# Performance work log

Measured on AMD Instinct MI355X. Metric: run time of the kernel, lower is better.

Reference implementation:

```python
import jax, jax.numpy as jnp
import numpy as np

D_MODEL = 1024
N_HEADS = 16
HEAD_DIM = D_MODEL // N_HEADS
B, S = 2, 2048


def setup_inputs() -> dict:
    key = jax.random.key(0)
    ks = jax.random.split(key, 6)
    w_scale = 1.0 / np.sqrt(D_MODEL)
    return {
        "query": jax.random.normal(ks[0], (B, S, D_MODEL), dtype=jnp.float32),
        "Wq": jax.random.normal(ks[1], (D_MODEL, D_MODEL), dtype=jnp.float32) * w_scale,
        "Wk": jax.random.normal(ks[2], (D_MODEL, D_MODEL), dtype=jnp.float32) * w_scale,
        "Wv": jax.random.normal(ks[3], (D_MODEL, D_MODEL), dtype=jnp.float32) * w_scale,
        "Wo": jax.random.normal(ks[4], (D_MODEL, D_MODEL), dtype=jnp.float32) * w_scale,
        "bo": jnp.zeros((D_MODEL,), dtype=jnp.float32),
    }


def reference(query, Wq, Wk, Wv, Wo, bo):
    # Self-attention: key = value = query (forward() defaults).
    b, t, _ = query.shape
    # Q/K/V projections (nn.Linear applies x @ W.T; weights here are stored as
    # [out, in] like torch, so project with W.T). Split into heads: [B,H,T,Dh].
    def proj(x, W):
        return (x @ W.T).reshape(b, t, N_HEADS, HEAD_DIM).transpose(0, 2, 1, 3)

    q = proj(query, Wq)
    k = proj(query, Wk)
    v = proj(query, Wv)

    scale = 1.0 / np.sqrt(HEAD_DIM)
    scores = jnp.einsum("bhqd,bhkd->bhqk", q, k) * scale  # [B,H,T,T]
    # Causal mask (is_causal=True, not cross-attention).
    causal = jnp.tril(jnp.ones((t, t), dtype=bool))
    scores = jnp.where(causal, scores, jnp.finfo(scores.dtype).min)
    weights = jax.nn.softmax(scores, axis=-1)
    out = jnp.einsum("bhqk,bhkd->bhqd", weights, v)  # [B,H,T,Dh]
    out = out.transpose(0, 2, 1, 3).reshape(b, t, D_MODEL)
    # Output projection with bias (dropout is identity in eval mode).
    return out @ Wo.T + bo
```

## Files before the change

### kernel.cpp

```cpp
#include <hip/hip_runtime.h>
#include <hip/hip_bf16.h>
#include <math.h>

typedef __attribute__((ext_vector_type(8))) short short8;
typedef __attribute__((ext_vector_type(4))) float floatx4;
typedef __attribute__((ext_vector_type(2))) _Float16 half2v;
typedef __attribute__((ext_vector_type(4))) _Float16 half4v;

#define MFMA_BF16_32(a, b, c) __builtin_amdgcn_mfma_f32_16x16x32_bf16(a, b, c, 0, 0, 0)
#define MFMA_F16_16(a, b, c) __builtin_amdgcn_mfma_f32_16x16x16f16(a, b, c, 0, 0, 0)

#define PIPE_BAR4() asm volatile("s_waitcnt vmcnt(4)\n\ts_barrier" ::: "memory")
#define PIPE_BAR0() asm volatile("s_waitcnt vmcnt(0)\n\ts_barrier" ::: "memory")

static constexpr int NH = 16;
static constexpr int Bb = 2;
static constexpr int Ss = 2048;
static constexpr int DM = 1024;

__device__ inline unsigned short f2bf(float f) {
    unsigned int u = __float_as_uint(f);
    u += 0x7fffu + ((u >> 16) & 1u);
    return (unsigned short)(u >> 16);
}

__device__ __forceinline__ half2v pkrtz(float a, float b) {
    return __builtin_bit_cast(half2v, __builtin_amdgcn_cvt_pkrtz(a, b));
}

__device__ __forceinline__ void gload_lds16(const unsigned short* g, unsigned short* l) {
    __builtin_amdgcn_global_load_lds(
        (const __attribute__((address_space(1))) unsigned int*)g,
        (__attribute__((address_space(3))) unsigned int*)l, 16, 0, 0);
}

__global__ void convert_all(const float* __restrict__ X, const float* __restrict__ w0,
                            const float* __restrict__ w1, const float* __restrict__ w2,
                            const float* __restrict__ w3, unsigned short* __restrict__ dstX,
                            unsigned short* __restrict__ dstW) {
    const int bid = blockIdx.x;
    const float* src;
    unsigned short* dst;
    int i;
    if (bid < 4096) {
        src = X; dst = dstX; i = bid * 256 + threadIdx.x;
    } else {
        const int w = (bid - 4096) >> 10;
        src = (w == 0) ? w0 : (w == 1) ? w1 : (w == 2) ? w2 : w3;
        dst = dstW + (size_t)w * 1048576;
        i = ((bid - 4096) & 1023) * 256 + threadIdx.x;
    }
    float4 v = ((const float4*)src)[i];
    ushort4 o;
    o.x = f2bf(v.x); o.y = f2bf(v.y); o.z = f2bf(v.z); o.w = f2bf(v.w);
    ((ushort4*)dst)[i] = o;
}

__global__ __launch_bounds__(256) void gemm_qkv(const unsigned short* __restrict__ A,
                                                const unsigned short* __restrict__ Bm,
                                                unsigned short* __restrict__ Qp,
                                                unsigned short* __restrict__ Kp,
                                                unsigned short* __restrict__ Vt) {
    __shared__ __align__(16) unsigned short As[2][4096];
    __shared__ __align__(16) unsigned short Bs[2][4096];
    const int K = 1024;
    const int tid = threadIdx.x;
    const int wave = tid >> 6, lane = tid & 63;
    const int quad = lane >> 4, l16 = lane & 15;
    const int wr = wave >> 1, wc = wave & 1;

    const int l = blockIdx.x;
    const int xcd = l & 7, slot = l >> 3;
    const int bx = (xcd & 3) * 8 + (slot & 7);
    const int by = (xcd >> 2) * 12 + (slot >> 3);
    const int bm = bx * 128;
    const int bn = by * 128;

    const int s0 = wave * 64 + lane;
    const int srow = s0 >> 2;
    const int scg = (s0 & 3) ^ ((srow >> 1) & 3);
    const unsigned short* gA0 = A + (size_t)(bm + srow) * K + scg * 8;
    const unsigned short* gB0 = Bm + (size_t)(bn + srow) * K + scg * 8;

    auto stage = [&](int k0, int buf) {
        gload_lds16(gA0 + k0, &As[buf][wave * 512]);
        gload_lds16(gA0 + (size_t)64 * K + k0, &As[buf][2048 + wave * 512]);
        gload_lds16(gB0 + k0, &Bs[buf][wave * 512]);
        gload_lds16(gB0 + (size_t)64 * K + k0, &Bs[buf][2048 + wave * 512]);
    };

    floatx4 acc[4][4];
#pragma unroll
    for (int i = 0; i < 4; i++)
#pragma unroll
        for (int j = 0; j < 4; j++) acc[i][j] = (floatx4)0.0f;

    stage(0, 0);
    int buf = 0;
    for (int k0 = 0; k0 < K; k0 += 32) {
        __syncthreads();
        if (k0 + 32 < K) stage(k0 + 32, buf ^ 1);
        short8 af[4];
#pragma unroll
        for (int im = 0; im < 4; im++) {
            const int frow = wr * 64 + im * 16 + l16;
            af[im] = *(const short8*)&As[buf][frow * 32 + ((quad ^ ((frow >> 1) & 3)) * 8)];
        }
#pragma unroll
        for (int jn = 0; jn < 4; jn++) {
            const int frow = wc * 64 + jn * 16 + l16;
            short8 bf = *(const short8*)&Bs[buf][frow * 32 + ((quad ^ ((frow >> 1) & 3)) * 8)];
#pragma unroll
            for (int im = 0; im < 4; im++) acc[im][jn] = MFMA_BF16_32(af[im], bf, acc[im][jn]);
        }
        buf ^= 1;
    }
    __syncthreads();

    unsigned short* LB = &As[0][0];

    if (by < 16) {
        unsigned short* dst = (by < 8) ? Qp : Kp;
        const int nb = (by & 7) * 128;
        const float scale = (by < 8) ? 0.125f : 1.0f;
#pragma unroll
        for (int hf = 0; hf < 2; ++hf) {
            if (wc == hf) {
#pragma unroll
                for (int im = 0; im < 4; im++)
#pragma unroll
                    for (int jn = 0; jn < 4; jn++) {
                        const int row = wr * 64 + im * 16 + quad * 4;
                        const int col = jn * 16 + l16;
#pragma unroll
                        for (int r = 0; r < 4; r++)
                            LB[(row + r) * 64 + col] = f2bf(acc[im][jn][r] * scale);
                    }
            }
            __syncthreads();
#pragma unroll
            for (int i = 0; i < 4; ++i) {
                const int flat = i * 256 + tid;
                const int row = flat >> 3, ch = flat & 7;
                short8 v = *(const short8*)&LB[row * 64 + ch * 8];
                *(short8*)&dst[(size_t)(bm + row) * 1024 + nb + hf * 64 + ch * 8] = v;
            }
            __syncthreads();
        }
    } else {
        _Float16* LF = (_Float16*)LB;
        const int dbase = (by - 16) * 128;
        const int bI = bm >> 11, sbase = bm & 2047;
#pragma unroll
        for (int hf = 0; hf < 2; ++hf) {
            if (wc == hf) {
#pragma unroll
                for (int im = 0; im < 4; im++)
#pragma unroll
                    for (int jn = 0; jn < 4; jn++) {
                        const int d64 = jn * 16 + l16;
                        const int sl = wr * 64 + im * 16 + quad * 4;
                        *(half2v*)&LF[d64 * 128 + sl] = pkrtz(acc[im][jn][0], acc[im][jn][1]);
                        *(half2v*)&LF[d64 * 128 + sl + 2] = pkrtz(acc[im][jn][2], acc[im][jn][3]);
                    }
            }
            __syncthreads();
#pragma unroll
            for (int i = 0; i < 4; ++i) {
                const int flat = i * 256 + tid;
                const int dr = flat >> 4, ch = flat & 15;
                short8 v = *(const short8*)&LF[dr * 128 + ch * 8];
                const int d = dbase + hf * 64 + dr;
                const int head = d >> 6, d64g = d & 63;
                *(short8*)&Vt[(((size_t)(bI * 16 + head)) * 64 + d64g) * 2048 + sbase + ch * 8] = v;
            }
            __syncthreads();
        }
    }
}

__global__ __launch_bounds__(256) void gemm_out(const unsigned short* __restrict__ A,
                                                const unsigned short* __restrict__ Bm,
                                                float* __restrict__ C,
                                                const float* __restrict__ bias) {
    __shared__ __align__(16) unsigned short As[2][8192];
    __shared__ __align__(16) unsigned short Bs[2][4096];
    const int K = 1024;
    const int tid = threadIdx.x;
    const int wave = tid >> 6, lane = tid & 63;
    const int quad = lane >> 4, l16 = lane & 15;

    const int l = blockIdx.x;
    const int xcd = l & 7, slot = l >> 3;
    const int bx = (xcd & 3) * 8 + (slot & 7);
    const int by = (xcd >> 2) * 8 + (slot >> 3);
    const int bm = bx * 128, bn = by * 64;

    const int s0 = wave * 64 + lane;
    const int srow = s0 >> 2;
    const int scg = (s0 & 3) ^ ((srow >> 1) & 3);
    const unsigned short* gA0 = A + (size_t)(bm + srow) * K + scg * 8;
    const unsigned short* gB0 = Bm + (size_t)(bn + srow) * K + scg * 8;

    auto stage = [&](int k0, int buf) {
#pragma unroll
        for (int kh = 0; kh < 2; ++kh) {
            gload_lds16(gA0 + k0 + kh * 32, &As[buf][kh * 4096 + wave * 512]);
            gload_lds16(gA0 + (size_t)64 * K + k0 + kh * 32,
                        &As[buf][kh * 4096 + 2048 + wave * 512]);
            gload_lds16(gB0 + k0 + kh * 32, &Bs[buf][kh * 2048 + wave * 512]);
        }
    };

    floatx4 acc[2][4];
#pragma unroll
    for (int i = 0; i < 2; i++)
#pragma unroll
        for (int j = 0; j < 4; j++) acc[i][j] = (floatx4)0.0f;

    stage(0, 0);
    int buf = 0;
    for (int k0 = 0; k0 < K; k0 += 64) {
        __syncthreads();
        if (k0 + 64 < K) stage(k0 + 64, buf ^ 1);
#pragma unroll
        for (int kh = 0; kh < 2; ++kh) {
            const int abase = kh * 4096, bbase = kh * 2048;
            short8 af[2];
#pragma unroll
            for (int im = 0; im < 2; im++) {
                const int frow = wave * 32 + im * 16 + l16;
                af[im] = *(const short8*)&As[buf][abase + frow * 32 +
                                                  ((quad ^ ((frow >> 1) & 3)) * 8)];
            }
#pragma unroll
            for (int jn = 0; jn < 4; jn++) {
                const int frow = jn * 16 + l16;
                short8 bf = *(const short8*)&Bs[buf][bbase + frow * 32 +
                                                     ((quad ^ ((frow >> 1) & 3)) * 8)];
#pragma unroll
                for (int im = 0; im < 2; im++) acc[im][jn] = MFMA_BF16_32(af[im], bf, acc[im][jn]);
            }
        }
        buf ^= 1;
    }

#pragma unroll
    for (int im = 0; im < 2; im++) {
#pragma unroll
        for (int jn = 0; jn < 4; jn++) {
            const int row0 = bm + wave * 32 + im * 16 + quad * 4;
            const int colg = bn + jn * 16 + l16;
            const float bv = bias[colg];
#pragma unroll
            for (int r = 0; r < 4; r++)
                C[(size_t)(row0 + r) * 1024 + colg] = acc[im][jn][r] + bv;
        }
    }
}

__global__ __launch_bounds__(256) void flash_attn(const unsigned short* __restrict__ Qp,
                                                  const unsigned short* __restrict__ Kp,
                                                  const _Float16* __restrict__ Vt,
                                                  unsigned short* __restrict__ Out) {
    __shared__ __align__(16) unsigned short Ks[3][4096];
    __shared__ __align__(16) _Float16 Vs[3][4096];
    const int lin = blockIdx.x;
    const int xcd = lin & 7, slot = lin >> 3;
    const int pair = xcd * 4 + ((slot >> 4) & 3);
    const int h = pair & 15, b = pair >> 4;
    const int qt0 = slot & 15;
    const int qt = ((slot >> 5) & 1) ? 15 - qt0 : qt0;

    const int tid = threadIdx.x, w = tid >> 6, lane = tid & 63;
    const int quad = lane >> 4, l16 = lane & 15;

    short8 qfA[2], qfB[2];
    {
        const unsigned short* qa =
            Qp + ((size_t)(b * 2048 + qt * 128 + w * 16 + l16) << 10) + h * 64 + quad * 8;
        qfA[0] = *(const short8*)qa;
        qfA[1] = *(const short8*)(qa + 32);
        const unsigned short* qb = qa + ((size_t)64 << 10);
        qfB[0] = *(const short8*)qb;
        qfB[1] = *(const short8*)(qb + 32);
    }

    const int t8 = tid >> 3;
    const int cg = (tid & 7) ^ (t8 & 7);
    const unsigned short* gK0 = Kp + ((size_t)(b * 2048 + t8) << 10) + h * 64 + cg * 8;
    const unsigned short* gK1 = gK0 + ((size_t)32 << 10);
    const _Float16* gV0 = Vt + ((size_t)((b * 16 + h) * 64 + t8) << 11) + cg * 8;
    const _Float16* gV1 = gV0 + ((size_t)32 << 11);
    unsigned short* ldsK = &Ks[0][0] + w * 512;
    _Float16* ldsV = &Vs[0][0] + w * 512;

    auto stage = [&](int kt, int buf) {
        const size_t ko = (size_t)kt << 16;
        const size_t vo = (size_t)kt << 6;
        gload_lds16(gK0 + ko, ldsK + buf * 4096);
        gload_lds16(gK1 + ko, ldsK + buf * 4096 + 2048);
        gload_lds16((const unsigned short*)(gV0 + vo), (unsigned short*)(ldsV + buf * 4096));
        gload_lds16((const unsigned short*)(gV1 + vo), (unsigned short*)(ldsV + buf * 4096 + 2048));
    };

    const int ktEnd = 2 * qt + 1;
    stage(0, 0);
    stage(1, 1);

    floatx4 accA[4], accB[4];
#pragma unroll
    for (int dt = 0; dt < 4; dt++) { accA[dt] = (floatx4)0.0f; accB[dt] = (floatx4)0.0f; }
    float lA = 0.0f, lB = 0.0f;
    const int qloc = w * 16 + l16;
    const int sw = l16 & 7;

    int buf = 0;
    for (int kt = 0; kt <= ktEnd; ++kt) {
        if (kt < ktEnd) { PIPE_BAR4(); } else { PIPE_BAR0(); }
        const int nbuf = (buf == 2) ? 0 : buf + 1;
        const int pbuf = (nbuf == 2) ? 0 : nbuf + 1;
        if (kt + 2 <= ktEnd) stage(kt + 2, pbuf);
        const bool aAct = (kt <= 2 * qt);
        const bool aDiag = (kt == 2 * qt);
        const bool bDiag = (kt == ktEnd);
        const unsigned short* KB = &Ks[buf][0];
        const _Float16* VB = &Vs[buf][0];

#pragma unroll
        for (int sc = 0; sc < 4; ++sc) {
            const int rowk = sc * 16 + l16;
            short8 kf0 = *(const short8*)&KB[rowk * 64 + ((quad ^ sw) * 8)];
            short8 kf1 = *(const short8*)&KB[rowk * 64 + (((4 + quad) ^ sw) * 8)];

            half4v pA, pB;
            if (aAct) {
                floatx4 sA = MFMA_BF16_32(kf0, qfA[0], (floatx4)(-2.0f));
                sA = MFMA_BF16_32(kf1, qfA[1], sA);
                float ps[4];
#pragma unroll
                for (int r = 0; r < 4; ++r) {
                    float e = __expf(sA[r]);
                    if (aDiag && (sc * 16 + quad * 4 + r > qloc)) e = 0.0f;
                    ps[r] = e;
                }
                lA += (ps[0] + ps[1]) + (ps[2] + ps[3]);
                pA = __builtin_shufflevector(pkrtz(ps[0], ps[1]), pkrtz(ps[2], ps[3]), 0, 1, 2, 3);
            }
            {
                floatx4 sB = MFMA_BF16_32(kf0, qfB[0], (floatx4)(-2.0f));
                sB = MFMA_BF16_32(kf1, qfB[1], sB);
                float ps[4];
#pragma unroll
                for (int r = 0; r < 4; ++r) {
                    float e = __expf(sB[r]);
                    if (bDiag && (sc * 16 + quad * 4 + r > qloc)) e = 0.0f;
                    ps[r] = e;
                }
                lB += (ps[0] + ps[1]) + (ps[2] + ps[3]);
                pB = __builtin_shufflevector(pkrtz(ps[0], ps[1]), pkrtz(ps[2], ps[3]), 0, 1, 2, 3);
            }

#pragma unroll
            for (int dt = 0; dt < 4; ++dt) {
                const int rowv = dt * 16 + l16;
                const int cgv = ((sc * 2 + (quad >> 1)) ^ sw);
                half4v vf = *(const half4v*)&VB[rowv * 64 + cgv * 8 + (quad & 1) * 4];
                if (aAct) accA[dt] = MFMA_F16_16(vf, pA, accA[dt]);
                accB[dt] = MFMA_F16_16(vf, pB, accB[dt]);
            }
        }
        buf = nbuf;
    }

    lA += __shfl_xor(lA, 16); lA += __shfl_xor(lA, 32);
    lB += __shfl_xor(lB, 16); lB += __shfl_xor(lB, 32);
    const float iA = 1.0f / lA;
    const float iB = 1.0f / lB;

    const size_t rowA = (size_t)(b * 2048 + qt * 128 + w * 16 + l16);
    const size_t rowB = rowA + 64;
#pragma unroll
    for (int dt = 0; dt < 4; ++dt) {
        const int col = h * 64 + dt * 16 + quad * 4;
        ushort4 oa, ob;
        oa.x = f2bf(accA[dt][0] * iA); oa.y = f2bf(accA[dt][1] * iA);
        oa.z = f2bf(accA[dt][2] * iA); oa.w = f2bf(accA[dt][3] * iA);
        ob.x = f2bf(accB[dt][0] * iB); ob.y = f2bf(accB[dt][1] * iB);
        ob.z = f2bf(accB[dt][2] * iB); ob.w = f2bf(accB[dt][3] * iB);
        *(ushort4*)&Out[rowA * 1024 + col] = oa;
        *(ushort4*)&Out[rowB * 1024 + col] = ob;
    }
}

extern "C" void kernel_launch(void* const* d_in, const int* in_sizes, int n_in,
                              void* d_out, int out_size, void* d_ws, size_t ws_size,
                              hipStream_t stream) {
    const float* X  = (const float*)d_in[0];
    const float* Wq = (const float*)d_in[1];
    const float* Wk = (const float*)d_in[2];
    const float* Wv = (const float*)d_in[3];
    const float* Wo = (const float*)d_in[4];
    const float* bo = (const float*)d_in[5];

    unsigned short* ws = (unsigned short*)d_ws;
    unsigned short* Xb   = ws;
    unsigned short* W4   = ws + (size_t)4194304;
    unsigned short* Wob  = W4 + (size_t)3145728;
    unsigned short* Qp   = ws + (size_t)8388608;
    unsigned short* Kp   = ws + (size_t)12582912;
    unsigned short* Vt   = ws + (size_t)16777216;
    unsigned short* At   = ws + (size_t)20971520;

    convert_all<<<8192, 256, 0, stream>>>(X, Wq, Wk, Wv, Wo, Xb, W4);

    gemm_qkv<<<768, 256, 0, stream>>>(Xb, W4, Qp, Kp, Vt);

    flash_attn<<<512, 256, 0, stream>>>(Qp, Kp, (const _Float16*)Vt, At);

    gemm_out<<<512, 256, 0, stream>>>(At, Wob, (float*)d_out, bo);
}
```

Measured before the change: 197.0 us.

## Replace LDS-staged QKV GEMM with single-wave register-direct 64x64 tiles

```diff
diff --git a/kernel.cpp b/kernel.cpp
--- a/kernel.cpp
+++ b/kernel.cpp
@@ -56,38 +56,37 @@
     ((ushort4*)dst)[i] = o;
 }
 
-__global__ __launch_bounds__(256) void gemm_qkv(const unsigned short* __restrict__ A,
-                                                const unsigned short* __restrict__ Bm,
-                                                unsigned short* __restrict__ Qp,
-                                                unsigned short* __restrict__ Kp,
-                                                unsigned short* __restrict__ Vt) {
-    __shared__ __align__(16) unsigned short As[2][4096];
-    __shared__ __align__(16) unsigned short Bs[2][4096];
+__global__ __launch_bounds__(64) void qkv_wave(const unsigned short* __restrict__ A,
+                                               const unsigned short* __restrict__ W,
+                                               unsigned short* __restrict__ Qp,
+                                               unsigned short* __restrict__ Kp,
+                                               unsigned short* __restrict__ Vt) {
+    __shared__ __align__(16) unsigned short T[64 * 68];
     const int K = 1024;
-    const int tid = threadIdx.x;
-    const int wave = tid >> 6, lane = tid & 63;
+    const int lane = threadIdx.x;
     const int quad = lane >> 4, l16 = lane & 15;
-    const int wr = wave >> 1, wc = wave & 1;
-
-    const int l = blockIdx.x;
-    const int xcd = l & 7, slot = l >> 3;
-    const int bx = (xcd & 3) * 8 + (slot & 7);
-    const int by = (xcd >> 2) * 12 + (slot >> 3);
-    const int bm = bx * 128;
-    const int bn = by * 128;
-
-    const int s0 = wave * 64 + lane;
-    const int srow = s0 >> 2;
-    const int scg = (s0 & 3) ^ ((srow >> 1) & 3);
-    const unsigned short* gA0 = A + (size_t)(bm + srow) * K + scg * 8;
-    const unsigned short* gB0 = Bm + (size_t)(bn + srow) * K + scg * 8;
-
-    auto stage = [&](int k0, int buf) {
-        gload_lds16(gA0 + k0, &As[buf][wave * 512]);
-        gload_lds16(gA0 + (size_t)64 * K + k0, &As[buf][2048 + wave * 512]);
-        gload_lds16(gB0 + k0, &Bs[buf][wave * 512]);
-        gload_lds16(gB0 + (size_t)64 * K + k0, &Bs[buf][2048 + wave * 512]);
-    };
+
+    const int lin = blockIdx.x;
+    int bm, bn;
+    const unsigned short *Ab, *Bb_;
+    const bool isV = (lin >= 2048);
+    if (!isV) {
+        const int xcd = lin & 7, slot = lin >> 3;
+        bm = ((xcd & 3) * 16 + (slot & 15)) * 64;
+        bn = ((xcd >> 2) * 16 + (slot >> 4)) * 64;
+        Ab = A;
+        Bb_ = W;
+    } else {
+        const int l2 = lin - 2048;
+        const int xcd = l2 & 7, slot = l2 >> 3;
+        bm = ((xcd & 3) * 4 + (slot >> 5)) * 64;
+        bn = ((xcd >> 2) * 32 + (slot & 31)) * 64;
+        Ab = W + (size_t)2048 * 1024;
+        Bb_ = A;
+    }
+
+    const unsigned short* pa = Ab + (size_t)(bm + l16) * K + quad * 8;
+    const unsigned short* pb = Bb_ + (size_t)(bn + l16) * K + quad * 8;
 
     floatx4 acc[4][4];
 #pragma unroll
@@ -95,86 +94,79 @@
 #pragma unroll
         for (int j = 0; j < 4; j++) acc[i][j] = (floatx4)0.0f;
 
-    stage(0, 0);
-    int buf = 0;
-    for (int k0 = 0; k0 < K; k0 += 32) {
-        __syncthreads();
-        if (k0 + 32 < K) stage(k0 + 32, buf ^ 1);
-        short8 af[4];
-#pragma unroll
-        for (int im = 0; im < 4; im++) {
-            const int frow = wr * 64 + im * 16 + l16;
-            af[im] = *(const short8*)&As[buf][frow * 32 + ((quad ^ ((frow >> 1) & 3)) * 8)];
-        }
-#pragma unroll
-        for (int jn = 0; jn < 4; jn++) {
-            const int frow = wc * 64 + jn * 16 + l16;
-            short8 bf = *(const short8*)&Bs[buf][frow * 32 + ((quad ^ ((frow >> 1) & 3)) * 8)];
-#pragma unroll
-            for (int im = 0; im < 4; im++) acc[im][jn] = MFMA_BF16_32(af[im], bf, acc[im][jn]);
-        }
-        buf ^= 1;
-    }
-    __syncthreads();
-
-    unsigned short* LB = &As[0][0];
-
-    if (by < 16) {
-        unsigned short* dst = (by < 8) ? Qp : Kp;
-        const int nb = (by & 7) * 128;
-        const float scale = (by < 8) ? 0.125f : 1.0f;
-#pragma unroll
-        for (int hf = 0; hf < 2; ++hf) {
-            if (wc == hf) {
-#pragma unroll
-                for (int im = 0; im < 4; im++)
-#pragma unroll
-                    for (int jn = 0; jn < 4; jn++) {
-                        const int row = wr * 64 + im * 16 + quad * 4;
-                        const int col = jn * 16 + l16;
-#pragma unroll
-                        for (int r = 0; r < 4; r++)
-                            LB[(row + r) * 64 + col] = f2bf(acc[im][jn][r] * scale);
-                    }
-            }
-            __syncthreads();
-#pragma unroll
-            for (int i = 0; i < 4; ++i) {
-                const int flat = i * 256 + tid;
-                const int row = flat >> 3, ch = flat & 7;
-                short8 v = *(const short8*)&LB[row * 64 + ch * 8];
-                *(short8*)&dst[(size_t)(bm + row) * 1024 + nb + hf * 64 + ch * 8] = v;
-            }
-            __syncthreads();
+    short8 af0[4], bf0[4], af1[4], bf1[4];
+#define LOADSET(AF, BF, KO)                                                      \
+    {                                                                            \
+        _Pragma("unroll") for (int i = 0; i < 4; i++)                            \
+            AF[i] = *(const short8*)(pa + (size_t)i * 16 * K + (KO));            \
+        _Pragma("unroll") for (int j = 0; j < 4; j++)                            \
+            BF[j] = *(const short8*)(pb + (size_t)j * 16 * K + (KO));            \
+    }
+#define MFMASET(AF, BF)                                                          \
+    {                                                                            \
+        _Pragma("unroll") for (int j = 0; j < 4; j++)                            \
+            _Pragma("unroll") for (int i = 0; i < 4; i++)                        \
+                acc[i][j] = MFMA_BF16_32(AF[i], BF[j], acc[i][j]);               \
+    }
+
+    LOADSET(af0, bf0, 0)
+#pragma unroll 4
+    for (int k0 = 0; k0 < 1024; k0 += 64) {
+        LOADSET(af1, bf1, k0 + 32)
+        MFMASET(af0, bf0)
+        if (k0 + 64 < 1024) LOADSET(af0, bf0, k0 + 64)
+        MFMASET(af1, bf1)
+    }
+#undef LOADSET
+#undef MFMASET
+
+    const float scale = (!isV && bn < 1024) ? 0.125f : 1.0f;
+#pragma unroll
+    for (int i = 0; i < 4; i++) {
+#pragma unroll
+        for (int j = 0; j < 4; j++) {
+            ushort4 pk;
+            if (isV) {
+                half2v h0 = pkrtz(acc[i][j][0], acc[i][j][1]);
+                half2v h1 = pkrtz(acc[i][j][2], acc[i][j][3]);
+                unsigned int u0 = __builtin_bit_cast(unsigned int, h0);
+                unsigned int u1 = __builtin_bit_cast(unsigned int, h1);
+                pk.x = (unsigned short)(u0 & 0xffff);
+                pk.y = (unsigned short)(u0 >> 16);
+                pk.z = (unsigned short)(u1 & 0xffff);
+                pk.w = (unsigned short)(u1 >> 16);
+            } else {
+                pk.x = f2bf(acc[i][j][0] * scale);
+                pk.y = f2bf(acc[i][j][1] * scale);
+                pk.z = f2bf(acc[i][j][2] * scale);
+                pk.w = f2bf(acc[i][j][3] * scale);
+            }
+            *(ushort4*)&T[(j * 16 + l16) * 68 + i * 16 + quad * 4] = pk;
+        }
+    }
+
+    const int ch = lane & 7;
+    if (!isV) {
+        unsigned short* dst = (bn < 1024) ? Qp : Kp;
+        const int colbase = (bn & 1023) + ch * 8;
+#pragma unroll
+        for (int it = 0; it < 8; ++it) {
+            const int m = it * 8 + (lane >> 3);
+            unsigned short tmp[8];
+#pragma unroll
+            for (int j = 0; j < 8; ++j) tmp[j] = T[(ch * 8 + j) * 68 + m];
+            *(short8*)&dst[(size_t)(bm + m) * 1024 + colbase] = *(short8*)tmp;
         }
     } else {
-        _Float16* LF = (_Float16*)LB;
-        const int dbase = (by - 16) * 128;
-        const int bI = bm >> 11, sbase = bm & 2047;
-#pragma unroll
-        for (int hf = 0; hf < 2; ++hf) {
-            if (wc == hf) {
-#pragma unroll
-                for (int im = 0; im < 4; im++)
-#pragma unroll
-                    for (int jn = 0; jn < 4; jn++) {
-                        const int d64 = jn * 16 + l16;
-                        const int sl = wr * 64 + im * 16 + quad * 4;
-                        *(half2v*)&LF[d64 * 128 + sl] = pkrtz(acc[im][jn][0], acc[im][jn][1]);
-                        *(half2v*)&LF[d64 * 128 + sl + 2] = pkrtz(acc[im][jn][2], acc[im][jn][3]);
-                    }
-            }
-            __syncthreads();
-#pragma unroll
-            for (int i = 0; i < 4; ++i) {
-                const int flat = i * 256 + tid;
-                const int dr = flat >> 4, ch = flat & 15;
-                short8 v = *(const short8*)&LF[dr * 128 + ch * 8];
-                const int d = dbase + hf * 64 + dr;
-                const int head = d >> 6, d64g = d & 63;
-                *(short8*)&Vt[(((size_t)(bI * 16 + head)) * 64 + d64g) * 2048 + sbase + ch * 8] = v;
-            }
-            __syncthreads();
+        const int bI = bn >> 11, sb = (bn & 2047) + ch * 8;
+        const size_t rowbase = (size_t)(bI * 16 + (bm >> 6)) * 64;
+#pragma unroll
+        for (int it = 0; it < 8; ++it) {
+            const int m = it * 8 + (lane >> 3);
+            unsigned short tmp[8];
+#pragma unroll
+            for (int j = 0; j < 8; ++j) tmp[j] = T[(ch * 8 + j) * 68 + m];
+            *(short8*)&Vt[(rowbase + m) * 2048 + sb] = *(short8*)tmp;
         }
     }
 }
@@ -414,7 +406,7 @@
 
     convert_all<<<8192, 256, 0, stream>>>(X, Wq, Wk, Wv, Wo, Xb, W4);
 
-    gemm_qkv<<<768, 256, 0, stream>>>(Xb, W4, Qp, Kp, Vt);
+    qkv_wave<<<3072, 64, 0, stream>>>(Xb, W4, Qp, Kp, Vt);
 
     flash_attn<<<512, 256, 0, stream>>>(Qp, Kp, (const _Float16*)Vt, At);
 
```

Result: slower. 248.7 us (+26.3%).
